# Performance work log

Measured on AMD Instinct MI355X. Metric: run time of the kernel, lower is better.

The kernel has to match this reference:

```python
import jax, jax.numpy as jnp
import numpy as np
from jax import lax

BATCH = 8192
HIDDEN = 128
N_POINTS = 8
MAX_STEPS = 8     # adaptive substep budget per output interval
RTOL, ATOL = 1e-3, 1e-4

# Dormand-Prince 5(4) tableau (FSAL)
A21 = 1/5
A31, A32 = 3/40, 9/40
A41, A42, A43 = 44/45, -56/15, 32/9
A51, A52, A53, A54 = 19372/6561, -25360/2187, 64448/6561, -212/729
A61, A62, A63, A64, A65 = 9017/3168, -355/33, 46732/5247, 49/176, -5103/18656
B1, B3, B4, B5, B6 = 35/384, 500/1113, 125/192, -2187/6784, 11/84
# error weights = b(5th) - b(4th)
E1 = 35/384 - 5179/57600
E3 = 500/1113 - 7571/16695
E4 = 125/192 - 393/640
E5 = -2187/6784 + 92097/339200
E6 = 11/84 - 187/2100
E7 = -1/40


def setup_inputs() -> dict:
    key = jax.random.key(0)
    ks = jax.random.split(key, 6)
    def xavier(k, fi, fo):
        return (jax.random.normal(k, (fi, fo)) * jnp.sqrt(2.0 / (fi + fo))).astype(jnp.float32)
    W1 = xavier(ks[0], 2, HIDDEN); b1 = jnp.zeros((HIDDEN,), jnp.float32)
    W2 = xavier(ks[1], HIDDEN, HIDDEN); b2 = jnp.zeros((HIDDEN,), jnp.float32)
    W3 = xavier(ks[2], HIDDEN, HIDDEN); b3 = jnp.zeros((HIDDEN,), jnp.float32)
    W4 = xavier(ks[3], HIDDEN, 2); b4 = jnp.zeros((2,), jnp.float32)
    x0 = jax.random.normal(ks[4], (BATCH, 2), jnp.float32)
    t = (jnp.arange(N_POINTS, dtype=jnp.float32) * 0.1)
    return {"x0": x0, "t": t, "W1": W1, "b1": b1, "W2": W2, "b2": b2,
            "W3": W3, "b3": b3, "W4": W4, "b4": b4}


def _odeint(x0, t, W1, b1, W2, b2, W3, b3, W4, b4):
    def f(y):  # autonomous dynamics: ODEFunc ignores t
        h = jax.nn.elu(y @ W1 + b1)
        h = jax.nn.elu(h @ W2 + b2)
        h = jax.nn.elu(h @ W3 + b3)
        return h @ W4 + b4

    def dopri5_step(y, h):
        k1 = f(y)
        k2 = f(y + h * (A21 * k1))
        k3 = f(y + h * (A31 * k1 + A32 * k2))
        k4 = f(y + h * (A41 * k1 + A42 * k2 + A43 * k3))
        k5 = f(y + h * (A51 * k1 + A52 * k2 + A53 * k3 + A54 * k4))
        k6 = f(y + h * (A61 * k1 + A62 * k2 + A63 * k3 + A64 * k4 + A65 * k5))
        y5 = y + h * (B1 * k1 + B3 * k3 + B4 * k4 + B5 * k5 + B6 * k6)
        k7 = f(y5)  # FSAL stage, used only for error estimate here
        err = h * (E1 * k1 + E3 * k3 + E4 * k4 + E5 * k5 + E6 * k6 + E7 * k7)
        tol = ATOL + RTOL * jnp.maximum(jnp.abs(y), jnp.abs(y5))
        err_norm = jnp.sqrt(jnp.mean((err / tol) ** 2))
        return y5, err_norm

    def solve_interval(carry, ts):
        y, h = carry
        t0, t1 = ts

        def body(c, _):
            y, tc, h = c
            remaining = t1 - tc
            done = remaining <= 1e-9
            h_eff = jnp.where(done, h, jnp.minimum(h, remaining))
            y5, err_norm = dopri5_step(y, h_eff)
            accept = (err_norm <= 1.0) & (~done)
            y = jnp.where(accept, y5, y)
            tc = jnp.where(accept, tc + h_eff, tc)
            factor = jnp.clip(0.9 * jnp.maximum(err_norm, 1e-10) ** (-0.2), 0.2, 10.0)
            h = jnp.where(done, h, h_eff * factor)
            return (y, tc, h), None

        (y, _, h), _ = lax.scan(body, (y, t0, h), None, length=MAX_STEPS)
        return (y, h), y

    h0 = (t[1] - t[0]) * 0.5
    (_, _), ys = lax.scan(solve_interval, (x0, h0), (t[:-1], t[1:]))
    return jnp.concatenate([x0[None], ys], axis=0)  # (n_points, batch, 2)


def reference(x0, t, W1, b1, W2, b2, W3, b3, W4, b4):
    return _odeint(x0, t, W1, b1, W2, b2, W3, b3, W4, b4)
```

## Files before the change

### kernel.cpp

```cpp
#include <hip/hip_runtime.h>
#include <stdint.h>

typedef unsigned int u32;
typedef unsigned long long u64;
typedef unsigned short u16;
typedef float f32x4 __attribute__((ext_vector_type(4)));
typedef float f32x2 __attribute__((ext_vector_type(2)));
typedef short short8 __attribute__((ext_vector_type(8)));
typedef unsigned int u32x2 __attribute__((ext_vector_type(2)));
typedef unsigned int u32x4 __attribute__((ext_vector_type(4)));

#define HID  128
#define MT   32
#define NWG  256
#define NTHR 512
#define LD   136

#define OFF_ROOT  0
#define OFF_LEAF  4096
#define OFF_WPACK 61440
#define OFF_W2TH  65536
#define OFF_W3TH  98304

constexpr float CA21 = (float)(1.0/5.0);
constexpr float CA31 = (float)(3.0/40.0),   CA32 = (float)(9.0/40.0);
constexpr float CA41 = (float)(44.0/45.0),  CA42 = (float)(-56.0/15.0), CA43 = (float)(32.0/9.0);
constexpr float CA51 = (float)(19372.0/6561.0), CA52 = (float)(-25360.0/2187.0);
constexpr float CA53 = (float)(64448.0/6561.0), CA54 = (float)(-212.0/729.0);
constexpr float CA61 = (float)(9017.0/3168.0),  CA62 = (float)(-355.0/33.0);
constexpr float CA63 = (float)(46732.0/5247.0), CA64 = (float)(49.0/176.0), CA65 = (float)(-5103.0/18656.0);
constexpr float CB1 = (float)(35.0/384.0), CB3 = (float)(500.0/1113.0), CB4 = (float)(125.0/192.0);
constexpr float CB5 = (float)(-2187.0/6784.0), CB6 = (float)(11.0/84.0);
constexpr float CE1 = (float)(35.0/384.0 - 5179.0/57600.0);
constexpr float CE3 = (float)(500.0/1113.0 - 7571.0/16695.0);
constexpr float CE4 = (float)(125.0/192.0 - 393.0/640.0);
constexpr float CE5 = (float)(-2187.0/6784.0 + 92097.0/339200.0);
constexpr float CE6 = (float)(11.0/84.0 - 187.0/2100.0);
constexpr float CE7 = (float)(-1.0/40.0);

template<int N> struct IC { static constexpr int v = N; };

__device__ __forceinline__ u16 f2bf(float x) {
  u32 u = __builtin_bit_cast(u32, x);
  u32 r = (u + 0x7FFFu + ((u >> 16) & 1u)) >> 16;
  return (u16)r;
}
__device__ __forceinline__ float eluf(float x) {
  return x > 0.f ? x : (__expf(x) - 1.f);
}
__device__ __forceinline__ u32 cvtpk(float a, float b) {
  u32 r; asm("v_cvt_pk_bf16_f32 %0, %1, %2" : "=v"(r) : "v"(a), "v"(b)); return r;
}

__global__ void prologue(const float* __restrict__ x0, const float* __restrict__ t,
                         const float* __restrict__ W1, const float* __restrict__ b1,
                         const float* __restrict__ W2, const float* __restrict__ b2,
                         const float* __restrict__ W3, const float* __restrict__ b3,
                         const float* __restrict__ W4, const float* __restrict__ b4,
                         float* __restrict__ ws, float* __restrict__ out)
{
  int gid = blockIdx.x * blockDim.x + threadIdx.x;
  out[gid] = x0[gid];
  {
    int k = gid >> 7, j = gid & 127;
    u16* w2th = (u16*)((char*)ws + OFF_W2TH);
    u16* w3th = (u16*)((char*)ws + OFF_W3TH);
    w2th[j*HID + k] = f2bf(W2[gid]);
    w3th[j*HID + k] = f2bf(W3[gid]);
  }
  float* wp = ws + OFF_WPACK/4;
  if (gid < 256) wp[gid] = W1[gid];
  if (gid < 128) {
    wp[256 + gid] = b1[gid];
    wp[384 + gid] = b2[gid];
    wp[512 + gid] = b3[gid];
  }
  if (gid < 2)  wp[640 + gid] = b4[gid];
  if (gid < 15360) ((u32*)ws)[gid] = 0u;
}

__global__ __launch_bounds__(NTHR, 2)
void solver(const float* __restrict__ x0, const float* __restrict__ t_arr,
            const float* __restrict__ W4g, float* __restrict__ ws,
            float* __restrict__ out)
{
  const int tid  = threadIdx.x;
  const int wg   = blockIdx.x;
  const int lane = tid & 63;
  const int wv   = tid >> 6;
  const int nl   = lane & 15;
  const int g    = lane >> 4;
  const int m    = tid >> 4;
  const int jc   = tid & 15;

  __shared__ __align__(16) u16 Ahi[2][MT][LD];
  __shared__ __align__(16) float Wsm[644];
  __shared__ __align__(16) float kSm[6][MT][2];
  __shared__ __align__(16) float yLm[MT][2];
  __shared__ __align__(16) float y5m[MT][2];
  __shared__ __align__(16) float pD[8][MT][2];
  __shared__ u32 bcF;
  __shared__ float bcH;

  {
    const float* wp = ws + OFF_WPACK/4;
    Wsm[tid] = wp[tid];
    if (tid < 132) Wsm[512 + tid] = wp[512 + tid];
  }
  float y0r = x0[wg*64 + m*2 + 0];
  float y1r = x0[wg*64 + m*2 + 1];
  if (jc == 0) { yLm[m][0] = y0r; yLm[m][1] = y1r; }

  const u16* w2th = (const u16*)((const char*)ws + OFF_W2TH);
  const u16* w3th = (const u16*)((const char*)ws + OFF_W3TH);
  short8 W2H[4], W3H[4];
  {
    const int nglob = wv*16 + nl;
#pragma unroll
    for (int ks = 0; ks < 4; ++ks) {
      int off = nglob*HID + ks*32 + g*8;
      W2H[ks] = *(const short8*)(w2th + off);
      W3H[ks] = *(const short8*)(w3th + off);
    }
  }
  float w4c[4][2];
#pragma unroll
  for (int r = 0; r < 4; ++r) {
    int n = wv*16 + g*4 + r;
    w4c[r][0] = W4g[n*2 + 0];
    w4c[r][1] = W4g[n*2 + 1];
  }
  __syncthreads();
  const f32x4 bv2 = *(const f32x4*)&Wsm[384 + wv*16 + g*4];
  const f32x4 bv3 = *(const f32x4*)&Wsm[512 + wv*16 + g*4];
  const float b40 = Wsm[640], b41 = Wsm[641];

  float khv[6][2];
  float y5r0 = 0.f, y5r1 = 0.f;

  float h = 0.5f * (t_arr[1] - t_arr[0]);
  float heff = h;

  auto phaseA = [&](auto SC) {
    constexpr int S = decltype(SC)::v;
    float ys0, ys1;
    if constexpr (S == 1) {
      ys0 = y0r; ys1 = y1r;
    } else {
      float kp0, kp1;
      if constexpr (S == 2) {
        kp0 = khv[0][0]; kp1 = khv[0][1];
      } else {
        kp0 = b40; kp1 = b41;
#pragma unroll
        for (int w = 0; w < 8; ++w) {
          f32x2 p = *(const f32x2*)&pD[w][m][0];
          kp0 += p[0]; kp1 += p[1];
        }
        khv[S-2][0] = kp0; khv[S-2][1] = kp1;
        if constexpr (S >= 4) {
          if (jc == 0) { kSm[S-2][m][0] = kp0; kSm[S-2][m][1] = kp1; }
        }
      }
      if constexpr (S == 2) {
        ys0 = fmaf(heff, CA21*kp0, y0r);
        ys1 = fmaf(heff, CA21*kp1, y1r);
      } else if constexpr (S == 3) {
        ys0 = fmaf(heff, CA31*khv[0][0] + CA32*kp0, y0r);
        ys1 = fmaf(heff, CA31*khv[0][1] + CA32*kp1, y1r);
      } else if constexpr (S == 4) {
        ys0 = fmaf(heff, CA41*khv[0][0] + CA42*khv[1][0] + CA43*kp0, y0r);
        ys1 = fmaf(heff, CA41*khv[0][1] + CA42*khv[1][1] + CA43*kp1, y1r);
      } else if constexpr (S == 5) {
        ys0 = fmaf(heff, CA51*khv[0][0] + CA52*khv[1][0] + CA53*khv[2][0] + CA54*kp0, y0r);
        ys1 = fmaf(heff, CA51*khv[0][1] + CA52*khv[1][1] + CA53*khv[2][1] + CA54*kp1, y1r);
      } else if constexpr (S == 6) {
        ys0 = fmaf(heff, CA61*khv[0][0] + CA62*khv[1][0] + CA63*khv[2][0] + CA64*khv[3][0] + CA65*kp0, y0r);
        ys1 = fmaf(heff, CA61*khv[0][1] + CA62*khv[1][1] + CA63*khv[2][1] + CA64*khv[3][1] + CA65*kp1, y1r);
      } else {
        ys0 = fmaf(heff, CB1*khv[0][0] + CB3*khv[2][0] + CB4*khv[3][0] + CB5*khv[4][0] + CB6*kp0, y0r);
        ys1 = fmaf(heff, CB1*khv[0][1] + CB3*khv[2][1] + CB4*khv[3][1] + CB5*khv[4][1] + CB6*kp1, y1r);
        y5r0 = ys0; y5r1 = ys1;
        if (jc == 0) { y5m[m][0] = ys0; y5m[m][1] = ys1; }
      }
    }
    const int j0 = jc * 8;
    f32x4 w0a = *(const f32x4*)&Wsm[j0],       w0b = *(const f32x4*)&Wsm[j0 + 4];
    f32x4 w1a = *(const f32x4*)&Wsm[128 + j0], w1b = *(const f32x4*)&Wsm[128 + j0 + 4];
    f32x4 ba  = *(const f32x4*)&Wsm[256 + j0], bb  = *(const f32x4*)&Wsm[256 + j0 + 4];
    float v0 = eluf(fmaf(ys1, w1a[0], fmaf(ys0, w0a[0], ba[0])));
    float v1 = eluf(fmaf(ys1, w1a[1], fmaf(ys0, w0a[1], ba[1])));
    float v2 = eluf(fmaf(ys1, w1a[2], fmaf(ys0, w0a[2], ba[2])));
    float v3 = eluf(fmaf(ys1, w1a[3], fmaf(ys0, w0a[3], ba[3])));
    float v4 = eluf(fmaf(ys1, w1b[0], fmaf(ys0, w0b[0], bb[0])));
    float v5 = eluf(fmaf(ys1, w1b[1], fmaf(ys0, w0b[1], bb[1])));
    float v6 = eluf(fmaf(ys1, w1b[2], fmaf(ys0, w0b[2], bb[2])));
    float v7 = eluf(fmaf(ys1, w1b[3], fmaf(ys0, w0b[3], bb[3])));
    u32x4 hp = {cvtpk(v0,v1), cvtpk(v2,v3), cvtpk(v4,v5), cvtpk(v6,v7)};
    *(u32x4*)&Ahi[0][m][j0] = hp;
  };

  auto mmL2 = [&]() {
    f32x4 a0[2];
    a0[0] = bv2; a0[1] = bv2;
#pragma unroll
    for (int ks = 0; ks < 4; ++ks)
#pragma unroll
      for (int mt = 0; mt < 2; ++mt) {
        short8 bh = *(const short8*)&Ahi[0][mt*16 + nl][ks*32 + g*8];
        a0[mt] = __builtin_amdgcn_mfma_f32_16x16x32_bf16(W2H[ks], bh, a0[mt], 0, 0, 0);
      }
    const int n0 = wv*16 + g*4;
#pragma unroll
    for (int mt = 0; mt < 2; ++mt) {
      float v0 = eluf(a0[mt][0]);
      float v1 = eluf(a0[mt][1]);
      float v2 = eluf(a0[mt][2]);
      float v3 = eluf(a0[mt][3]);
      u32x2 hp = {cvtpk(v0, v1), cvtpk(v2, v3)};
      *(u32x2*)&Ahi[1][mt*16 + nl][n0] = hp;
    }
  };

  auto mmL3 = [&]() {
    f32x4 a0[2];
    a0[0] = bv3; a0[1] = bv3;
#pragma unroll
    for (int ks = 0; ks < 4; ++ks)
#pragma unroll
      for (int mt = 0; mt < 2; ++mt) {
        short8 bh = *(const short8*)&Ahi[1][mt*16 + nl][ks*32 + g*8];
        a0[mt] = __builtin_amdgcn_mfma_f32_16x16x32_bf16(W3H[ks], bh, a0[mt], 0, 0, 0);
      }
#pragma unroll
    for (int mt = 0; mt < 2; ++mt) {
      float v0 = eluf(a0[mt][0]);
      float v1 = eluf(a0[mt][1]);
      float v2 = eluf(a0[mt][2]);
      float v3 = eluf(a0[mt][3]);
      float p0 = v0*w4c[0][0] + v1*w4c[1][0] + v2*w4c[2][0] + v3*w4c[3][0];
      float p1 = v0*w4c[0][1] + v1*w4c[1][1] + v2*w4c[2][1] + v3*w4c[3][1];
      p0 += __shfl_xor(p0, 16); p0 += __shfl_xor(p0, 32);
      p1 += __shfl_xor(p1, 16); p1 += __shfl_xor(p1, 32);
      if (lane < 16) {
        f32x2 pp = {p0, p1};
        *(f32x2*)&pD[wv][mt*16 + lane][0] = pp;
      }
    }
  };

  for (int iv = 0; iv < 7; ++iv) {
    const float t1 = t_arr[iv + 1];
    float tc = t_arr[iv];
    for (int s = 0; s < 8; ++s) {
      const int step = iv*8 + s;
      float rem = t1 - tc;
      if (rem <= 1e-9f) break;
      heff = fminf(h, rem);

      if (iv == 0 && s == 0) {
        phaseA(IC<1>{}); __syncthreads();
        mmL2(); __syncthreads();
        mmL3(); __syncthreads();
        float kp0 = b40, kp1 = b41;
#pragma unroll
        for (int w = 0; w < 8; ++w) {
          f32x2 p = *(const f32x2*)&pD[w][m][0];
          kp0 += p[0]; kp1 += p[1];
        }
        khv[0][0] = kp0; khv[0][1] = kp1;
        if (jc == 0) { kSm[0][m][0] = kp0; kSm[0][m][1] = kp1; }
      }
      phaseA(IC<2>{}); __syncthreads(); mmL2(); __syncthreads(); mmL3(); __syncthreads();
      phaseA(IC<3>{}); __syncthreads(); mmL2(); __syncthreads(); mmL3(); __syncthreads();
      phaseA(IC<4>{}); __syncthreads(); mmL2(); __syncthreads(); mmL3(); __syncthreads();
      phaseA(IC<5>{}); __syncthreads(); mmL2(); __syncthreads(); mmL3(); __syncthreads();
      phaseA(IC<6>{}); __syncthreads(); mmL2(); __syncthreads(); mmL3(); __syncthreads();
      phaseA(IC<7>{}); __syncthreads(); mmL2(); __syncthreads(); mmL3(); __syncthreads();

      if (wv == 0) {
        int em = lane >> 1, ec = lane & 1;
        float kp = ec ? b41 : b40;
#pragma unroll
        for (int w = 0; w < 8; ++w) kp += pD[w][em][ec];
        float e = heff * (CE1*kSm[0][em][ec] + CE3*kSm[2][em][ec] + CE4*kSm[3][em][ec]
                        + CE5*kSm[4][em][ec] + CE6*kSm[5][em][ec] + CE7*kp);
        float tol = 1e-4f + 1e-3f * fmaxf(fabsf(yLm[em][ec]), fabsf(y5m[em][ec]));
        float rr = e / tol;
        float es = rr * rr;
#pragma unroll
        for (int mk = 1; mk < 64; mk <<= 1) es += __shfl_xor(es, mk);
        if (lane == 0) {
          if (!(es < 1e9f)) es = 1e9f;
          u64 q = (u64)(es * 1024.0f);
          u64 add = (q << 10) | 1ULL;
          u64* leaf = (u64*)((char*)ws + OFF_LEAF + ((size_t)step*16 + (wg & 15))*64);
          u64 old = __hip_atomic_fetch_add(leaf, add, __ATOMIC_ACQ_REL, __HIP_MEMORY_SCOPE_AGENT);
          if ((old & 0x3FFULL) == 15ULL) {
            u64 tot = old + add;
            u64 radd = ((tot >> 10) << 10) | 1ULL;
            u64* rootp = (u64*)((char*)ws + OFF_ROOT + (size_t)step*64);
            __hip_atomic_fetch_add(rootp, radd, __ATOMIC_ACQ_REL, __HIP_MEMORY_SCOPE_AGENT);
          }
        }
      }
      float k7p0 = b40, k7p1 = b41;
#pragma unroll
      for (int w = 0; w < 8; ++w) {
        f32x2 p = *(const f32x2*)&pD[w][m][0];
        k7p0 += p[0]; k7p1 += p[1];
      }
      if (tid == 0) {
        u64* rootp = (u64*)((char*)ws + OFF_ROOT + (size_t)step*64);
        u64 v;
        while (((v = __hip_atomic_load(rootp, __ATOMIC_ACQUIRE, __HIP_MEMORY_SCOPE_AGENT)) & 0x3FFULL) != 16ULL)
          __builtin_amdgcn_s_sleep(1);
        float sum = (float)(v >> 10) * (1.0f/1024.0f);
        float err_norm = sqrtf(sum * (1.0f/16384.f));
        bool acc = (err_norm <= 1.0f);
        float factor = fminf(10.f, fmaxf(0.2f, 0.9f * powf(fmaxf(err_norm, 1e-10f), -0.2f)));
        bcF = acc ? 1u : 0u;
        bcH = heff * factor;
      }
      __syncthreads();
      {
        bool acc = bcF != 0u;
        if (acc) {
          y0r = y5r0; y1r = y5r1;
          khv[0][0] = k7p0; khv[0][1] = k7p1;
          if (jc == 0) {
            kSm[0][m][0] = k7p0; kSm[0][m][1] = k7p1;
            yLm[m][0] = y5r0;    yLm[m][1] = y5r1;
          }
          tc += heff;
        }
        h = bcH;
      }
    }
    if (jc == 0) {
      f32x2 yo = {y0r, y1r};
      *(f32x2*)&out[(size_t)(iv + 1) * 16384 + wg*64 + m*2] = yo;
    }
  }
}

extern "C" void kernel_launch(void* const* d_in, const int* in_sizes, int n_in,
                              void* d_out, int out_size, void* d_ws, size_t ws_size,
                              hipStream_t stream)
{
  const float* x0 = (const float*)d_in[0];
  const float* t  = (const float*)d_in[1];
  const float* W1 = (const float*)d_in[2];
  const float* b1 = (const float*)d_in[3];
  const float* W2 = (const float*)d_in[4];
  const float* b2 = (const float*)d_in[5];
  const float* W3 = (const float*)d_in[6];
  const float* b3 = (const float*)d_in[7];
  const float* W4 = (const float*)d_in[8];
  const float* b4 = (const float*)d_in[9];
  float* out = (float*)d_out;
  float* ws  = (float*)d_ws;

  prologue<<<64, 256, 0, stream>>>(x0, t, W1, b1, W2, b2, W3, b3, W4, b4, ws, out);
  solver<<<NWG, NTHR, 0, stream>>>(x0, t, W4, ws, out);
}
```

Before: 173.3 us.

## Halve workgroup to 4 waves with two N-tiles each; spin-flag broadcast

After: 172.1 us. Within noise of the previous version (-0.7%).

```diff
diff --git a/kernel.cpp b/kernel.cpp
--- a/kernel.cpp
+++ b/kernel.cpp
@@ -13,7 +13,7 @@
 #define HID  128
 #define MT   32
 #define NWG  256
-#define NTHR 512
+#define NTHR 256
 #define LD   136
 
 #define OFF_ROOT  0
@@ -90,49 +90,59 @@
   const int wv   = tid >> 6;
   const int nl   = lane & 15;
   const int g    = lane >> 4;
-  const int m    = tid >> 4;
-  const int jc   = tid & 15;
+  const int m    = tid >> 3;
+  const int jc   = tid & 7;
 
   __shared__ __align__(16) u16 Ahi[2][MT][LD];
   __shared__ __align__(16) float Wsm[644];
   __shared__ __align__(16) float kSm[6][MT][2];
   __shared__ __align__(16) float yLm[MT][2];
   __shared__ __align__(16) float y5m[MT][2];
-  __shared__ __align__(16) float pD[8][MT][2];
-  __shared__ u32 bcF;
-  __shared__ float bcH;
+  __shared__ __align__(16) float pD[4][MT][2];
+  __shared__ u32 flagL;
+  __shared__ u32 bcFl;
+  __shared__ float bcHl;
 
   {
     const float* wp = ws + OFF_WPACK/4;
     Wsm[tid] = wp[tid];
+    Wsm[256 + tid] = wp[256 + tid];
     if (tid < 132) Wsm[512 + tid] = wp[512 + tid];
   }
+  if (tid == 0) flagL = 0u;
   float y0r = x0[wg*64 + m*2 + 0];
   float y1r = x0[wg*64 + m*2 + 1];
   if (jc == 0) { yLm[m][0] = y0r; yLm[m][1] = y1r; }
 
   const u16* w2th = (const u16*)((const char*)ws + OFF_W2TH);
   const u16* w3th = (const u16*)((const char*)ws + OFF_W3TH);
-  short8 W2H[4], W3H[4];
-  {
-    const int nglob = wv*16 + nl;
+  short8 W2H[2][4], W3H[2][4];
+#pragma unroll
+  for (int nt = 0; nt < 2; ++nt) {
+    const int nglob = (wv*2 + nt)*16 + nl;
 #pragma unroll
     for (int ks = 0; ks < 4; ++ks) {
       int off = nglob*HID + ks*32 + g*8;
-      W2H[ks] = *(const short8*)(w2th + off);
-      W3H[ks] = *(const short8*)(w3th + off);
-    }
-  }
-  float w4c[4][2];
-#pragma unroll
-  for (int r = 0; r < 4; ++r) {
-    int n = wv*16 + g*4 + r;
-    w4c[r][0] = W4g[n*2 + 0];
-    w4c[r][1] = W4g[n*2 + 1];
-  }
+      W2H[nt][ks] = *(const short8*)(w2th + off);
+      W3H[nt][ks] = *(const short8*)(w3th + off);
+    }
+  }
+  float w4c[2][4][2];
+#pragma unroll
+  for (int nt = 0; nt < 2; ++nt)
+#pragma unroll
+    for (int r = 0; r < 4; ++r) {
+      int n = (wv*2 + nt)*16 + g*4 + r;
+      w4c[nt][r][0] = W4g[n*2 + 0];
+      w4c[nt][r][1] = W4g[n*2 + 1];
+    }
   __syncthreads();
-  const f32x4 bv2 = *(const f32x4*)&Wsm[384 + wv*16 + g*4];
-  const f32x4 bv3 = *(const f32x4*)&Wsm[512 + wv*16 + g*4];
+  f32x4 bv2[2], bv3[2];
+#pragma unroll
+  for (int nt = 0; nt < 2; ++nt) {
+    bv2[nt] = *(const f32x4*)&Wsm[384 + (wv*2 + nt)*16 + g*4];
+    bv3[nt] = *(const f32x4*)&Wsm[512 + (wv*2 + nt)*16 + g*4];
+  }
   const float b40 = Wsm[640], b41 = Wsm[641];
 
   float khv[6][2];
@@ -153,7 +163,7 @@
       } else {
         kp0 = b40; kp1 = b41;
 #pragma unroll
-        for (int w = 0; w < 8; ++w) {
+        for (int w = 0; w < 4; ++w) {
           f32x2 p = *(const f32x2*)&pD[w][m][0];
           kp0 += p[0]; kp1 += p[1];
         }
@@ -184,62 +194,80 @@
         if (jc == 0) { y5m[m][0] = ys0; y5m[m][1] = ys1; }
       }
     }
-    const int j0 = jc * 8;
-    f32x4 w0a = *(const f32x4*)&Wsm[j0],       w0b = *(const f32x4*)&Wsm[j0 + 4];
-    f32x4 w1a = *(const f32x4*)&Wsm[128 + j0], w1b = *(const f32x4*)&Wsm[128 + j0 + 4];
-    f32x4 ba  = *(const f32x4*)&Wsm[256 + j0], bb  = *(const f32x4*)&Wsm[256 + j0 + 4];
-    float v0 = eluf(fmaf(ys1, w1a[0], fmaf(ys0, w0a[0], ba[0])));
-    float v1 = eluf(fmaf(ys1, w1a[1], fmaf(ys0, w0a[1], ba[1])));
-    float v2 = eluf(fmaf(ys1, w1a[2], fmaf(ys0, w0a[2], ba[2])));
-    float v3 = eluf(fmaf(ys1, w1a[3], fmaf(ys0, w0a[3], ba[3])));
-    float v4 = eluf(fmaf(ys1, w1b[0], fmaf(ys0, w0b[0], bb[0])));
-    float v5 = eluf(fmaf(ys1, w1b[1], fmaf(ys0, w0b[1], bb[1])));
-    float v6 = eluf(fmaf(ys1, w1b[2], fmaf(ys0, w0b[2], bb[2])));
-    float v7 = eluf(fmaf(ys1, w1b[3], fmaf(ys0, w0b[3], bb[3])));
-    u32x4 hp = {cvtpk(v0,v1), cvtpk(v2,v3), cvtpk(v4,v5), cvtpk(v6,v7)};
-    *(u32x4*)&Ahi[0][m][j0] = hp;
+    const int j0 = jc * 16;
+    u32 hp[8];
+#pragma unroll
+    for (int b = 0; b < 4; ++b) {
+      f32x4 w0 = *(const f32x4*)&Wsm[j0 + b*4];
+      f32x4 w1 = *(const f32x4*)&Wsm[128 + j0 + b*4];
+      f32x4 bb = *(const f32x4*)&Wsm[256 + j0 + b*4];
+      float v0 = eluf(fmaf(ys1, w1[0], fmaf(ys0, w0[0], bb[0])));
+      float v1 = eluf(fmaf(ys1, w1[1], fmaf(ys0, w0[1], bb[1])));
+      float v2 = eluf(fmaf(ys1, w1[2], fmaf(ys0, w0[2], bb[2])));
+      float v3 = eluf(fmaf(ys1, w1[3], fmaf(ys0, w0[3], bb[3])));
+      hp[b*2 + 0] = cvtpk(v0, v1);
+      hp[b*2 + 1] = cvtpk(v2, v3);
+    }
+    u32x4 pa = {hp[0], hp[1], hp[2], hp[3]};
+    u32x4 pb = {hp[4], hp[5], hp[6], hp[7]};
+    *(u32x4*)&Ahi[0][m][j0]     = pa;
+    *(u32x4*)&Ahi[0][m][j0 + 8] = pb;
   };
 
   auto mmL2 = [&]() {
-    f32x4 a0[2];
-    a0[0] = bv2; a0[1] = bv2;
+    f32x4 acc[2][2];
+#pragma unroll
+    for (int mt = 0; mt < 2; ++mt)
+#pragma unroll
+      for (int nt = 0; nt < 2; ++nt) acc[mt][nt] = bv2[nt];
 #pragma unroll
     for (int ks = 0; ks < 4; ++ks)
 #pragma unroll
       for (int mt = 0; mt < 2; ++mt) {
         short8 bh = *(const short8*)&Ahi[0][mt*16 + nl][ks*32 + g*8];
-        a0[mt] = __builtin_amdgcn_mfma_f32_16x16x32_bf16(W2H[ks], bh, a0[mt], 0, 0, 0);
-      }
-    const int n0 = wv*16 + g*4;
-#pragma unroll
-    for (int mt = 0; mt < 2; ++mt) {
-      float v0 = eluf(a0[mt][0]);
-      float v1 = eluf(a0[mt][1]);
-      float v2 = eluf(a0[mt][2]);
-      float v3 = eluf(a0[mt][3]);
-      u32x2 hp = {cvtpk(v0, v1), cvtpk(v2, v3)};
-      *(u32x2*)&Ahi[1][mt*16 + nl][n0] = hp;
-    }
+#pragma unroll
+        for (int nt = 0; nt < 2; ++nt)
+          acc[mt][nt] = __builtin_amdgcn_mfma_f32_16x16x32_bf16(W2H[nt][ks], bh, acc[mt][nt], 0, 0, 0);
+      }
+#pragma unroll
+    for (int mt = 0; mt < 2; ++mt)
+#pragma unroll
+      for (int nt = 0; nt < 2; ++nt) {
+        float v0 = eluf(acc[mt][nt][0]);
+        float v1 = eluf(acc[mt][nt][1]);
+        float v2 = eluf(acc[mt][nt][2]);
+        float v3 = eluf(acc[mt][nt][3]);
+        u32x2 hp = {cvtpk(v0, v1), cvtpk(v2, v3)};
+        *(u32x2*)&Ahi[1][mt*16 + nl][(wv*2 + nt)*16 + g*4] = hp;
+      }
   };
 
   auto mmL3 = [&]() {
-    f32x4 a0[2];
-    a0[0] = bv3; a0[1] = bv3;
+    f32x4 acc[2][2];
+#pragma unroll
+    for (int mt = 0; mt < 2; ++mt)
+#pragma unroll
+      for (int nt = 0; nt < 2; ++nt) acc[mt][nt] = bv3[nt];
 #pragma unroll
     for (int ks = 0; ks < 4; ++ks)
 #pragma unroll
       for (int mt = 0; mt < 2; ++mt) {
         short8 bh = *(const short8*)&Ahi[1][mt*16 + nl][ks*32 + g*8];
-        a0[mt] = __builtin_amdgcn_mfma_f32_16x16x32_bf16(W3H[ks], bh, a0[mt], 0, 0, 0);
+#pragma unroll
+        for (int nt = 0; nt < 2; ++nt)
+          acc[mt][nt] = __builtin_amdgcn_mfma_f32_16x16x32_bf16(W3H[nt][ks], bh, acc[mt][nt], 0, 0, 0);
       }
 #pragma unroll
     for (int mt = 0; mt < 2; ++mt) {
-      float v0 = eluf(a0[mt][0]);
-      float v1 = eluf(a0[mt][1]);
-      float v2 = eluf(a0[mt][2]);
-      float v3 = eluf(a0[mt][3]);
-      float p0 = v0*w4c[0][0] + v1*w4c[1][0] + v2*w4c[2][0] + v3*w4c[3][0];
-      float p1 = v0*w4c[0][1] + v1*w4c[1][1] + v2*w4c[2][1] + v3*w4c[3][1];
+      float p0 = 0.f, p1 = 0.f;
+#pragma unroll
+      for (int nt = 0; nt < 2; ++nt)
+#pragma unroll
+        for (int r = 0; r < 4; ++r) {
+          float v = eluf(acc[mt][nt][r]);
+          p0 = fmaf(v, w4c[nt][r][0], p0);
+          p1 = fmaf(v, w4c[nt][r][1], p1);
+        }
       p0 += __shfl_xor(p0, 16); p0 += __shfl_xor(p0, 32);
       p1 += __shfl_xor(p1, 16); p1 += __shfl_xor(p1, 32);
       if (lane < 16) {
@@ -264,7 +292,7 @@
         mmL3(); __syncthreads();
         float kp0 = b40, kp1 = b41;
 #pragma unroll
-        for (int w = 0; w < 8; ++w) {
+        for (int w = 0; w < 4; ++w) {
           f32x2 p = *(const f32x2*)&pD[w][m][0];
           kp0 += p[0]; kp1 += p[1];
         }
@@ -282,7 +310,7 @@
         int em = lane >> 1, ec = lane & 1;
         float kp = ec ? b41 : b40;
 #pragma unroll
-        for (int w = 0; w < 8; ++w) kp += pD[w][em][ec];
+        for (int w = 0; w < 4; ++w) kp += pD[w][em][ec];
         float e = heff * (CE1*kSm[0][em][ec] + CE3*kSm[2][em][ec] + CE4*kSm[3][em][ec]
                         + CE5*kSm[4][em][ec] + CE6*kSm[5][em][ec] + CE7*kp);
         float tol = 1e-4f + 1e-3f * fmaxf(fabsf(yLm[em][ec]), fabsf(y5m[em][ec]));
@@ -306,7 +334,7 @@
       }
       float k7p0 = b40, k7p1 = b41;
 #pragma unroll
-      for (int w = 0; w < 8; ++w) {
+      for (int w = 0; w < 4; ++w) {
         f32x2 p = *(const f32x2*)&pD[w][m][0];
         k7p0 += p[0]; k7p1 += p[1];
       }
@@ -319,12 +347,14 @@
         float err_norm = sqrtf(sum * (1.0f/16384.f));
         bool acc = (err_norm <= 1.0f);
         float factor = fminf(10.f, fmaxf(0.2f, 0.9f * powf(fmaxf(err_norm, 1e-10f), -0.2f)));
-        bcF = acc ? 1u : 0u;
-        bcH = heff * factor;
-      }
-      __syncthreads();
+        bcFl = acc ? 1u : 0u;
+        bcHl = heff * factor;
+        __hip_atomic_store(&flagL, (u32)(step + 1), __ATOMIC_RELEASE, __HIP_MEMORY_SCOPE_WORKGROUP);
+      }
+      while (__hip_atomic_load(&flagL, __ATOMIC_ACQUIRE, __HIP_MEMORY_SCOPE_WORKGROUP) != (u32)(step + 1))
+        __builtin_amdgcn_s_sleep(1);
       {
-        bool acc = bcF != 0u;
+        bool acc = bcFl != 0u;
         if (acc) {
           y0r = y5r0; y1r = y5r1;
           khv[0][0] = k7p0; khv[0][1] = k7p1;
@@ -334,7 +364,7 @@
           }
           tc += heff;
         }
-        h = bcH;
+        h = bcHl;
       }
     }
     if (jc == 0) {
```
